# Optimization experiments

Measured on AMD Instinct MI355X. Metric: run time of the kernel, lower is better.

## Reference

```python
import jax, jax.numpy as jnp
import numpy as np

N = 100000      # nodes
E = 1600000     # edges (avg degree 16)
F_IN = 128      # node feature dim
F_OUT = 128     # GCN output dim


def setup_inputs() -> dict:
    key = jax.random.key(0)
    ks = jax.random.split(key, 11)
    s = 0.05  # weight scale to keep activations sane
    return {
        "x": jax.random.normal(ks[0], (N, F_IN), jnp.float32),
        "edge_index": jax.random.randint(ks[1], (2, E), 0, N, jnp.int32),
        "W": jax.random.normal(ks[2], (F_IN, F_OUT), jnp.float32) * s,
        "p": jax.random.normal(ks[3], (F_IN,), jnp.float32),
        "w_ih": jax.random.normal(ks[4], (3 * F_OUT, F_IN), jnp.float32) * s,
        "w_hh": jax.random.normal(ks[5], (3 * F_OUT, F_OUT), jnp.float32) * s,
        "b_ih": jax.random.normal(ks[6], (3 * F_OUT,), jnp.float32) * s,
        "b_hh": jax.random.normal(ks[7], (3 * F_OUT,), jnp.float32) * s,
        "conv_bias": jax.random.normal(ks[8], (F_OUT,), jnp.float32) * s,
        "lin_w": jax.random.normal(ks[9], (1, F_OUT), jnp.float32) * s,
        "lin_b": jax.random.normal(ks[10], (1,), jnp.float32) * s,
    }


def reference(x, edge_index, W, p, w_ih, w_hh, b_ih, b_hh, conv_bias, lin_w, lin_b):
    n_nodes = x.shape[0]
    k, H = W.shape  # k = F_IN rows, H = F_OUT hidden size

    # --- TopK summarize: pick k nodes, gate by tanh(score) -> X_tilde [k, F_IN]
    scores = x @ p / jnp.linalg.norm(p)
    top_vals, top_idx = jax.lax.top_k(scores, k)
    x_tilde = x[top_idx] * jnp.tanh(top_vals)[:, None]

    # --- one GRU step evolving W (hidden state = rows of W)
    gi = x_tilde @ w_ih.T + b_ih   # [k, 3H]
    gh = W @ w_hh.T + b_hh         # [k, 3H]
    r = jax.nn.sigmoid(gi[:, :H] + gh[:, :H])
    z = jax.nn.sigmoid(gi[:, H:2 * H] + gh[:, H:2 * H])
    n = jnp.tanh(gi[:, 2 * H:] + r * gh[:, 2 * H:])
    W_new = (1.0 - z) * n + z * W  # [F_IN, F_OUT]

    # --- GCN conv with fixed W: sym-normalized adjacency with self loops
    row, col = edge_index[0], edge_index[1]
    deg = jax.ops.segment_sum(jnp.ones_like(row, dtype=x.dtype), col,
                              num_segments=n_nodes) + 1.0  # +1 for self loop
    dinv = jax.lax.rsqrt(deg)
    xw = x @ W_new                                   # [N, F_OUT]
    coef = dinv[row] * dinv[col]                     # [E]
    agg = jax.ops.segment_sum(xw[row] * coef[:, None], col, num_segments=n_nodes)
    agg = agg + xw * (dinv * dinv)[:, None] + conv_bias  # self-loop term + bias

    # --- head: ReLU + Linear(F_OUT, 1)
    h = jax.nn.relu(agg)
    return h @ lin_w.T + lin_b  # [N, 1]
```

## Files before the change

kernel.cpp:

```cpp
#include <hip/hip_runtime.h>
#include <math.h>

#define N_NODES 100000
#define N_EDGES 1600000
#define F 128

#define BSH 9
#define NBUCK 196
#define PB_EDGES 4096

typedef unsigned int u32;
typedef unsigned long long u64;
typedef unsigned short u16;
typedef __attribute__((ext_vector_type(8))) short short8;
typedef __attribute__((ext_vector_type(4))) float floatx4;


__device__ __forceinline__ u32 key_of(float s) {
    u32 u = __float_as_uint(s);
    return (u & 0x80000000u) ? ~u : (u | 0x80000000u);
}

__device__ __forceinline__ float wave_reduce(float v) {
    #pragma unroll
    for (int off = 32; off > 0; off >>= 1) v += __shfl_down(v, off, 64);
    return v;
}

__device__ __forceinline__ u16 f2bf(float f) {
    u32 u = __float_as_uint(f);
    u += 0x7fffu + ((u >> 16) & 1u);
    return (u16)(u >> 16);
}


__global__ void k_scores(const float* __restrict__ x, const float* __restrict__ p,
                         float* __restrict__ scores, u32* __restrict__ hist16) {
    int node = blockIdx.x * 4 + (threadIdx.x >> 6);
    int lane = threadIdx.x & 63;
    if (node >= N_NODES) return;
    float2 xv = *(const float2*)&x[(size_t)node * F + lane * 2];
    float2 pv = *(const float2*)&p[lane * 2];
    float d = xv.x * pv.x + xv.y * pv.y;
    d = wave_reduce(d);
    if (lane == 0) {
        scores[node] = d;
        atomicAdd(&hist16[key_of(d) >> 16], 1u);
    }
}


__global__ __launch_bounds__(1024) void k_scan16(const u32* __restrict__ hist16,
                                                 u32* __restrict__ state) {
    __shared__ u32 a[1024];
    int t = threadIdx.x;
    const uint4* h4 = (const uint4*)hist16;
    u32 local = 0;
    #pragma unroll
    for (int i = 0; i < 16; i++) {
        uint4 v = h4[t * 16 + i];
        local += v.x + v.y + v.z + v.w;
    }
    a[t] = local;
    __syncthreads();
    for (int off = 1; off < 1024; off <<= 1) {
        u32 add = (t + off < 1024) ? a[t + off] : 0u;
        __syncthreads();
        a[t] += add;
        __syncthreads();
    }
    u32 S_above = (t == 1023) ? 0u : a[t + 1];
    if (S_above < 128u && a[t] >= 128u) {
        u32 cum = S_above;
        for (int v = t * 64 + 63; v >= t * 64; v--) {
            cum += hist16[v];
            if (cum >= 128u) { state[0] = (u32)v; break; }
        }
    }
}

__global__ void k_collect16(const float* __restrict__ scores, u32* __restrict__ state,
                            u32* __restrict__ cand) {
    u32 T = state[0] << 16;
    int i = blockIdx.x * blockDim.x + threadIdx.x;
    if (i < N_NODES) {
        if (key_of(scores[i]) >= T) {
            u32 pos = atomicAdd(&state[2], 1u);
            if (pos < 2048u) cand[pos] = (u32)i;
        }
    }
}

__global__ void k_assemble16(const float* __restrict__ scores, const float* __restrict__ p,
                             const u32* __restrict__ state, const u32* __restrict__ cand,
                             u32* __restrict__ top_idx, float* __restrict__ gate) {
    __shared__ u32 ci[2048];
    __shared__ float csc[2048];
    __shared__ float s_inv;
    int t = threadIdx.x;
    if (t < 64) {
        float2 pv = *(const float2*)&p[t * 2];
        float d = pv.x * pv.x + pv.y * pv.y;
        d = wave_reduce(d);
        if (t == 0) s_inv = rsqrtf(d);
    }
    u32 nc = state[2]; if (nc > 2048u) nc = 2048u;
    for (u32 i = t; i < nc; i += 256) { u32 ix = cand[i]; ci[i] = ix; csc[i] = scores[ix]; }
    __syncthreads();
    for (u32 i = t; i < nc; i += 256) {
        u32 myk = key_of(csc[i]);
        u32 myi = ci[i];
        int rank = 0;
        for (u32 j = 0; j < nc; j++) {
            u32 ok = key_of(csc[j]);
            rank += (int)((ok > myk) || (ok == myk && ci[j] < myi));
        }
        if (rank < 128) {
            top_idx[rank] = myi;
            gate[rank] = tanhf(csc[i] * s_inv);
        }
    }
}


__global__ __launch_bounds__(256) void k_ggemm(const float* __restrict__ x,
                                               const float* __restrict__ W,
                                               const float* __restrict__ w_ih,
                                               const float* __restrict__ w_hh,
                                               const u32* __restrict__ top_idx,
                                               const float* __restrict__ gate,
                                               float* __restrict__ G) {
    __shared__ float As[32][128];
    __shared__ float Bs[64][131];
    int t = threadIdx.x;
    int k0 = blockIdx.x * 32;
    int by = blockIdx.y;
    int j0 = by * 64;
    bool is_gi = (by < 6);
    #pragma unroll
    for (int i = 0; i < 4; i++) {
        int l = t + i * 256;
        int row = l >> 5, c4 = l & 31;
        float4 v;
        if (is_gi) {
            u32 idx = top_idx[k0 + row];
            float gt = gate[k0 + row];
            v = *(const float4*)&x[(size_t)idx * F + c4 * 4];
            v.x *= gt; v.y *= gt; v.z *= gt; v.w *= gt;
        } else {
            v = *(const float4*)&W[(k0 + row) * F + c4 * 4];
        }
        *(float4*)&As[row][c4 * 4] = v;
    }
    const float* mat = is_gi ? w_ih : w_hh;
    int jbase = is_gi ? j0 : (j0 - 384);
    #pragma unroll
    for (int i = 0; i < 8; i++) {
        int l = t + i * 256;
        int row = l >> 5, c4 = l & 31;
        float4 v = *(const float4*)&mat[(jbase + row) * F + c4 * 4];
        Bs[row][c4 * 4 + 0] = v.x; Bs[row][c4 * 4 + 1] = v.y;
        Bs[row][c4 * 4 + 2] = v.z; Bs[row][c4 * 4 + 3] = v.w;
    }
    __syncthreads();
    int ty = t >> 5, tx = t & 31;
    float acc[4][2] = {};
    #pragma unroll 4
    for (int f = 0; f < 128; f++) {
        float b0 = Bs[tx * 2][f], b1 = Bs[tx * 2 + 1][f];
        #pragma unroll
        for (int i = 0; i < 4; i++) {
            float a = As[ty * 4 + i][f];
            acc[i][0] += a * b0;
            acc[i][1] += a * b1;
        }
    }
    #pragma unroll
    for (int i = 0; i < 4; i++) {
        int k = k0 + ty * 4 + i;
        G[(size_t)k * 768 + j0 + tx * 2 + 0] = acc[i][0];
        G[(size_t)k * 768 + j0 + tx * 2 + 1] = acc[i][1];
    }
}


__global__ void k_gate(const float* __restrict__ G, const float* __restrict__ W,
                       const float* __restrict__ b_ih, const float* __restrict__ b_hh,
                       float* __restrict__ Wnew, u16* __restrict__ Bfrag) {
    int idx = blockIdx.x * blockDim.x + threadIdx.x;
    int k = idx >> 7, h = idx & 127;
    const float* gk = &G[(size_t)k * 768];
    float gir = gk[h]       + b_ih[h];
    float giz = gk[128 + h] + b_ih[128 + h];
    float gin = gk[256 + h] + b_ih[256 + h];
    float ghr = gk[384 + h] + b_hh[h];
    float ghz = gk[512 + h] + b_hh[128 + h];
    float ghn = gk[640 + h] + b_hh[256 + h];
    float wv  = W[k * F + h];
    float rg = 1.0f / (1.0f + expf(-(gir + ghr)));
    float z  = 1.0f / (1.0f + expf(-(giz + ghz)));
    float n  = tanhf(gin + rg * ghn);
    float val = (1.0f - z) * n + z * wv;
    Wnew[k * F + h] = val;
    int nb = h >> 4, kc = k >> 5, q = (k >> 3) & 3, m = h & 15, jj = k & 7;
    Bfrag[(((nb * 4 + kc) * 64) + q * 16 + m) * 8 + jj] = f2bf(val);
}


__global__ void k_bhist(const int* __restrict__ ei, u32* __restrict__ bhist) {
    __shared__ u32 h[NBUCK];
    int t = threadIdx.x;
    for (int i = t; i < NBUCK; i += 256) h[i] = 0u;
    __syncthreads();
    for (int e = blockIdx.x * blockDim.x + t; e < N_EDGES; e += gridDim.x * blockDim.x)
        atomicAdd(&h[((u32)ei[N_EDGES + e]) >> BSH], 1u);
    __syncthreads();
    for (int i = t; i < NBUCK; i += 256) if (h[i]) atomicAdd(&bhist[i], h[i]);
}

__global__ void k_bscan(const u32* __restrict__ bhist, u32* __restrict__ bbase,
                        u32* __restrict__ gcur) {
    __shared__ u32 s[256];
    int t = threadIdx.x;
    u32 v = (t < NBUCK) ? bhist[t] : 0u;
    s[t] = v;
    __syncthreads();
    for (int off = 1; off < 256; off <<= 1) {
        u32 add = (t >= off) ? s[t - off] : 0u;
        __syncthreads();
        s[t] += add;
        __syncthreads();
    }
    u32 excl = s[t] - v;
    if (t < NBUCK) { bbase[t] = excl; gcur[t] = excl; }
    if (t == 0) bbase[NBUCK] = N_EDGES;
}

__global__ void k_part(const int* __restrict__ ei, u32* __restrict__ gcur,
                       u64* __restrict__ pairs) {
    __shared__ u32 lh[NBUCK];
    __shared__ u32 lbase[NBUCK];
    int t = threadIdx.x;
    int e0 = blockIdx.x * PB_EDGES;
    int e1 = e0 + PB_EDGES; if (e1 > N_EDGES) e1 = N_EDGES;
    for (int i = t; i < NBUCK; i += 256) lh[i] = 0u;
    __syncthreads();
    for (int e = e0 + t; e < e1; e += 256)
        atomicAdd(&lh[((u32)ei[N_EDGES + e]) >> BSH], 1u);
    __syncthreads();
    for (int b = t; b < NBUCK; b += 256) {
        u32 c = lh[b];
        lbase[b] = c ? atomicAdd(&gcur[b], c) : 0u;
        lh[b] = 0u;
    }
    __syncthreads();
    for (int e = e0 + t; e < e1; e += 256) {
        u32 d = (u32)ei[N_EDGES + e];
        u32 b = d >> BSH;
        u32 pos = lbase[b] + atomicAdd(&lh[b], 1u);
        pairs[pos] = ((u64)d << 32) | (u32)ei[e];
    }
}

__global__ __launch_bounds__(256) void k_csr(const u64* __restrict__ pairs,
                                             const u32* __restrict__ bbase,
                                             u32* __restrict__ offs,
                                             float* __restrict__ dinv,
                                             u32* __restrict__ ebuf) {
    __shared__ u32 h[512];
    __shared__ u32 sc[512];
    int b = blockIdx.x, t = threadIdx.x;
    u32 lo = (u32)b << BSH;
    u32 base = bbase[b], end = bbase[b + 1];
    for (int i = t; i < 512; i += 256) h[i] = 0u;
    __syncthreads();
    for (u32 i = base + t; i < end; i += 256) {
        u32 dl = (u32)(pairs[i] >> 32) - lo;
        atomicAdd(&h[dl], 1u);
    }
    __syncthreads();
    for (int i = t; i < 512; i += 256) sc[i] = h[i];
    __syncthreads();
    for (int off = 1; off < 512; off <<= 1) {
        int i0 = t, i1 = t + 256;
        u32 v0 = (i0 >= off) ? sc[i0 - off] : 0u;
        u32 v1 = (i1 >= off) ? sc[i1 - off] : 0u;
        __syncthreads();
        sc[i0] += v0; sc[i1] += v1;
        __syncthreads();
    }
    int nn = N_NODES - (int)lo; if (nn > 512) nn = 512;
    for (int i = t; i < nn; i += 256) {
        u32 c = h[i];
        offs[lo + i] = base + (sc[i] - c);
        dinv[lo + i] = rsqrtf((float)c + 1.0f);
    }
    for (int i = t; i < 512; i += 256) sc[i] -= h[i];
    __syncthreads();
    for (u32 i = base + t; i < end; i += 256) {
        u64 pr = pairs[i];
        u32 dl = (u32)(pr >> 32) - lo;
        u32 pos = base + atomicAdd(&sc[dl], 1u);
        ebuf[pos] = (u32)pr;
    }
    if (b == 0 && t == 0) offs[N_NODES] = N_EDGES;
}


__global__ __launch_bounds__(256) void k_gemm(const float* __restrict__ x,
                                              const u16* __restrict__ Bfrag,
                                              u16* __restrict__ xwh) {
    __shared__ __align__(16) u16 As[8192];
    __shared__ __align__(16) u16 Bs[16384];
    int t = threadIdx.x;
    int r0 = blockIdx.x * 64;
    #pragma unroll
    for (int i = 0; i < 8; i++) {
        int l = t + i * 256;
        int row = l >> 5, c4 = l & 31;
        int f0 = c4 * 4;
        float4 v = {0.f, 0.f, 0.f, 0.f};
        if (r0 + row < N_NODES) v = *(const float4*)&x[(size_t)(r0 + row) * F + f0];
        int widx = (((row >> 4) * 4 + (f0 >> 5)) * 64 + ((f0 >> 3) & 3) * 16 + (row & 15)) * 8
                   + (f0 & 7);
        ushort4 s4;
        s4.x = f2bf(v.x); s4.y = f2bf(v.y); s4.z = f2bf(v.z); s4.w = f2bf(v.w);
        *(ushort4*)&As[widx] = s4;
    }
    #pragma unroll
    for (int i = 0; i < 8; i++) {
        int idx = t + i * 256;
        ((uint4*)Bs)[idx] = ((const uint4*)Bfrag)[idx];
    }
    __syncthreads();

    int wv = t >> 6, lane = t & 63;
    floatx4 acc[8] = {};
    #pragma unroll
    for (int kc = 0; kc < 4; kc++) {
        short8 a = *(const short8*)&As[((wv * 4 + kc) * 64 + lane) * 8];
        #pragma unroll
        for (int nb = 0; nb < 8; nb++) {
            short8 b = *(const short8*)&Bs[((nb * 4 + kc) * 64 + lane) * 8];
            acc[nb] = __builtin_amdgcn_mfma_f32_16x16x32_bf16(a, b, acc[nb], 0, 0, 0);
        }
    }
    int q = lane >> 4, m = lane & 15;
    #pragma unroll
    for (int nb = 0; nb < 8; nb++) {
        #pragma unroll
        for (int reg = 0; reg < 4; reg++) {
            int grow = r0 + wv * 16 + q * 4 + reg;
            if (grow < N_NODES)
                xwh[(size_t)grow * F + nb * 16 + m] = f2bf(acc[nb][reg]);
        }
    }
}


__global__ void k_gather(const u32* __restrict__ xw32, const u32* __restrict__ offs,
                         const u32* __restrict__ ebuf, const float* __restrict__ dinv,
                         const float* __restrict__ conv_bias, const float* __restrict__ lin_w,
                         const float* __restrict__ lin_b, float* __restrict__ out) {
    int c = blockIdx.x * 4 + (threadIdx.x >> 6);
    if (c >= N_NODES) return;
    int lane = threadIdx.x & 63;
    u32 jbeg = offs[c], jend = offs[c + 1];
    float ax0 = 0.f, ax1 = 0.f, ax2 = 0.f, ax3 = 0.f;
    float ay0 = 0.f, ay1 = 0.f, ay2 = 0.f, ay3 = 0.f;
    u32 j = jbeg;
    for (; j + 8 <= jend; j += 8) {
        u32 r[8], b[8];
        float w[8];
        #pragma unroll
        for (int i = 0; i < 8; i++) r[i] = ebuf[j + i];
        #pragma unroll
        for (int i = 0; i < 8; i++) w[i] = dinv[r[i]];
        #pragma unroll
        for (int i = 0; i < 8; i++) b[i] = xw32[(size_t)r[i] * 64 + lane];
        ax0 += w[0] * __uint_as_float(b[0] << 16); ay0 += w[0] * __uint_as_float(b[0] & 0xffff0000u);
        ax1 += w[1] * __uint_as_float(b[1] << 16); ay1 += w[1] * __uint_as_float(b[1] & 0xffff0000u);
        ax2 += w[2] * __uint_as_float(b[2] << 16); ay2 += w[2] * __uint_as_float(b[2] & 0xffff0000u);
        ax3 += w[3] * __uint_as_float(b[3] << 16); ay3 += w[3] * __uint_as_float(b[3] & 0xffff0000u);
        ax0 += w[4] * __uint_as_float(b[4] << 16); ay0 += w[4] * __uint_as_float(b[4] & 0xffff0000u);
        ax1 += w[5] * __uint_as_float(b[5] << 16); ay1 += w[5] * __uint_as_float(b[5] & 0xffff0000u);
        ax2 += w[6] * __uint_as_float(b[6] << 16); ay2 += w[6] * __uint_as_float(b[6] & 0xffff0000u);
        ax3 += w[7] * __uint_as_float(b[7] << 16); ay3 += w[7] * __uint_as_float(b[7] & 0xffff0000u);
    }
    for (; j < jend; j++) {
        u32 r = ebuf[j];
        float wv = dinv[r];
        u32 b = xw32[(size_t)r * 64 + lane];
        ax0 += wv * __uint_as_float(b << 16);
        ay0 += wv * __uint_as_float(b & 0xffff0000u);
    }
    float accx = (ax0 + ax1) + (ax2 + ax3);
    float accy = (ay0 + ay1) + (ay2 + ay3);
    float dc = dinv[c];
    u32 sbits = xw32[(size_t)c * 64 + lane];
    float slo = __uint_as_float(sbits << 16);
    float shi = __uint_as_float(sbits & 0xffff0000u);
    accx = dc * accx + dc * dc * slo + conv_bias[lane * 2];
    accy = dc * accy + dc * dc * shi + conv_bias[lane * 2 + 1];
    float hx = fmaxf(accx, 0.f), hy = fmaxf(accy, 0.f);
    float part = hx * lin_w[lane * 2] + hy * lin_w[lane * 2 + 1];
    part = wave_reduce(part);
    if (lane == 0) out[c] = part + lin_b[0];
}


extern "C" void kernel_launch(void* const* d_in, const int* in_sizes, int n_in,
                              void* d_out, int out_size, void* d_ws, size_t ws_size,
                              hipStream_t stream) {
    const float* x         = (const float*)d_in[0];
    const int*   ei        = (const int*)  d_in[1];
    const float* W         = (const float*)d_in[2];
    const float* p         = (const float*)d_in[3];
    const float* w_ih      = (const float*)d_in[4];
    const float* w_hh      = (const float*)d_in[5];
    const float* b_ih      = (const float*)d_in[6];
    const float* b_hh      = (const float*)d_in[7];
    const float* conv_bias = (const float*)d_in[8];
    const float* lin_w     = (const float*)d_in[9];
    const float* lin_b     = (const float*)d_in[10];
    float* out = (float*)d_out;

    u32*   w  = (u32*)d_ws;
    float* wf = (float*)d_ws;

    const size_t SCORES_W = 0;
    const size_t DINV_W   = 100096;
    const size_t OFFS_W   = 200192;
    const size_t HIST16_W = 300288;
    const size_t STATE_W  = 365824;
    const size_t CAND_W   = 365840;
    const size_t TOPI_W   = 367888;
    const size_t GATE_W   = 368016;
    const size_t WNEW_W   = 368144;
    const size_t BFRAG_W  = 384528;
    const size_t BHIST_W  = 392720;
    const size_t BBASE_W  = 392976;
    const size_t GCUR_W   = 393232;
    const size_t PAIRS_W  = 393488;
    const size_t EBUF_W   = 3593488;
    const size_t XW_W     = 5193488;

    float* scores  = wf + SCORES_W;
    float* dinv    = wf + DINV_W;
    u32*   offs    = w  + OFFS_W;
    u32*   hist16  = w  + HIST16_W;
    u32*   state   = w  + STATE_W;
    u32*   cand    = w  + CAND_W;
    u32*   top_idx = w  + TOPI_W;
    float* gate    = wf + GATE_W;
    float* Wnew    = wf + WNEW_W;
    u16*   Bfrag   = (u16*)(w + BFRAG_W);
    u32*   bhist   = w  + BHIST_W;
    u32*   bbase   = w  + BBASE_W;
    u32*   gcur    = w  + GCUR_W;
    u64*   pairs   = (u64*)(w + PAIRS_W);
    float* G       = wf + PAIRS_W;
    u32*   ebuf    = w  + EBUF_W;
    u16*   xwh     = (u16*)(w + XW_W);
    u32*   xw32    = w + XW_W;

    hipMemsetAsync(hist16, 0, (65536 + 8) * sizeof(u32), stream);
    hipMemsetAsync(bhist, 0, NBUCK * sizeof(u32), stream);

    k_scores<<<25000, 256, 0, stream>>>(x, p, scores, hist16);
    k_scan16<<<1, 1024, 0, stream>>>(hist16, state);
    k_collect16<<<392, 256, 0, stream>>>(scores, state, cand);
    k_assemble16<<<1, 256, 0, stream>>>(scores, p, state, cand, top_idx, gate);
    k_ggemm<<<dim3(4, 12), 256, 0, stream>>>(x, W, w_ih, w_hh, top_idx, gate, G);
    k_gate<<<64, 256, 0, stream>>>(G, W, b_ih, b_hh, Wnew, Bfrag);

    k_gemm<<<1563, 256, 0, stream>>>(x, Bfrag, xwh);

    k_bhist<<<392, 256, 0, stream>>>(ei, bhist);
    k_bscan<<<1, 256, 0, stream>>>(bhist, bbase, gcur);
    k_part<<<(N_EDGES + PB_EDGES - 1) / PB_EDGES, 256, 0, stream>>>(ei, gcur, pairs);
    k_csr<<<NBUCK, 256, 0, stream>>>(pairs, bbase, offs, dinv, ebuf);

    k_gather<<<25000, 256, 0, stream>>>(xw32, offs, ebuf, dinv, conv_bias, lin_w,
                                        lin_b, out);
}
```

Before: 363.6 us.

## Pack edge pairs into 32 bits, split gather wave across two edges, merge memsets

Edge partition pairs are now packed into 32 bits (9-bit local destination plus 17-bit source) instead of 64-bit words, halving the traffic of writing and reading the pair buffer in the CSR build. The gather kernel now processes two edges at once per wave, with each half-wave loading 8 bytes per lane per row and the halves combined by a cross-half shuffle. This is meant to issue fewer, wider memory requests. The workspace layout is reordered so the two histogram memsets merge into one call. The packing relies on node ids fitting in 17 bits.

```diff
diff --git a/kernel.cpp b/kernel.cpp
--- a/kernel.cpp
+++ b/kernel.cpp
@@ -10,7 +10,6 @@
 #define PB_EDGES 4096
 
 typedef unsigned int u32;
-typedef unsigned long long u64;
 typedef unsigned short u16;
 typedef __attribute__((ext_vector_type(8))) short short8;
 typedef __attribute__((ext_vector_type(4))) float floatx4;
@@ -32,6 +31,9 @@
     u += 0x7fffu + ((u >> 16) & 1u);
     return (u16)(u >> 16);
 }
+
+__device__ __forceinline__ float bflo(u32 b) { return __uint_as_float(b << 16); }
+__device__ __forceinline__ float bfhi(u32 b) { return __uint_as_float(b & 0xffff0000u); }
 
 
 __global__ void k_scores(const float* __restrict__ x, const float* __restrict__ p,
@@ -237,7 +239,7 @@
 }
 
 __global__ void k_part(const int* __restrict__ ei, u32* __restrict__ gcur,
-                       u64* __restrict__ pairs) {
+                       u32* __restrict__ pairs) {
     __shared__ u32 lh[NBUCK];
     __shared__ u32 lbase[NBUCK];
     int t = threadIdx.x;
@@ -258,11 +260,11 @@
         u32 d = (u32)ei[N_EDGES + e];
         u32 b = d >> BSH;
         u32 pos = lbase[b] + atomicAdd(&lh[b], 1u);
-        pairs[pos] = ((u64)d << 32) | (u32)ei[e];
-    }
-}
-
-__global__ __launch_bounds__(256) void k_csr(const u64* __restrict__ pairs,
+        pairs[pos] = ((d & 511u) << 17) | (u32)ei[e];
+    }
+}
+
+__global__ __launch_bounds__(256) void k_csr(const u32* __restrict__ pairs,
                                              const u32* __restrict__ bbase,
                                              u32* __restrict__ offs,
                                              float* __restrict__ dinv,
@@ -274,10 +276,8 @@
     u32 base = bbase[b], end = bbase[b + 1];
     for (int i = t; i < 512; i += 256) h[i] = 0u;
     __syncthreads();
-    for (u32 i = base + t; i < end; i += 256) {
-        u32 dl = (u32)(pairs[i] >> 32) - lo;
-        atomicAdd(&h[dl], 1u);
-    }
+    for (u32 i = base + t; i < end; i += 256)
+        atomicAdd(&h[pairs[i] >> 17], 1u);
     __syncthreads();
     for (int i = t; i < 512; i += 256) sc[i] = h[i];
     __syncthreads();
@@ -298,10 +298,9 @@
     for (int i = t; i < 512; i += 256) sc[i] -= h[i];
     __syncthreads();
     for (u32 i = base + t; i < end; i += 256) {
-        u64 pr = pairs[i];
-        u32 dl = (u32)(pr >> 32) - lo;
-        u32 pos = base + atomicAdd(&sc[dl], 1u);
-        ebuf[pos] = (u32)pr;
+        u32 pr = pairs[i];
+        u32 pos = base + atomicAdd(&sc[pr >> 17], 1u);
+        ebuf[pos] = pr & 0x1ffffu;
     }
     if (b == 0 && t == 0) offs[N_NODES] = N_EDGES;
 }
@@ -365,45 +364,51 @@
     int c = blockIdx.x * 4 + (threadIdx.x >> 6);
     if (c >= N_NODES) return;
     int lane = threadIdx.x & 63;
+    int half = lane >> 5, sub = lane & 31;
     u32 jbeg = offs[c], jend = offs[c + 1];
-    float ax0 = 0.f, ax1 = 0.f, ax2 = 0.f, ax3 = 0.f;
-    float ay0 = 0.f, ay1 = 0.f, ay2 = 0.f, ay3 = 0.f;
+    float ax = 0.f, ay = 0.f, az = 0.f, aw = 0.f;
     u32 j = jbeg;
     for (; j + 8 <= jend; j += 8) {
-        u32 r[8], b[8];
-        float w[8];
-        #pragma unroll
-        for (int i = 0; i < 8; i++) r[i] = ebuf[j + i];
-        #pragma unroll
-        for (int i = 0; i < 8; i++) w[i] = dinv[r[i]];
-        #pragma unroll
-        for (int i = 0; i < 8; i++) b[i] = xw32[(size_t)r[i] * 64 + lane];
-        ax0 += w[0] * __uint_as_float(b[0] << 16); ay0 += w[0] * __uint_as_float(b[0] & 0xffff0000u);
-        ax1 += w[1] * __uint_as_float(b[1] << 16); ay1 += w[1] * __uint_as_float(b[1] & 0xffff0000u);
-        ax2 += w[2] * __uint_as_float(b[2] << 16); ay2 += w[2] * __uint_as_float(b[2] & 0xffff0000u);
-        ax3 += w[3] * __uint_as_float(b[3] << 16); ay3 += w[3] * __uint_as_float(b[3] & 0xffff0000u);
-        ax0 += w[4] * __uint_as_float(b[4] << 16); ay0 += w[4] * __uint_as_float(b[4] & 0xffff0000u);
-        ax1 += w[5] * __uint_as_float(b[5] << 16); ay1 += w[5] * __uint_as_float(b[5] & 0xffff0000u);
-        ax2 += w[6] * __uint_as_float(b[6] << 16); ay2 += w[6] * __uint_as_float(b[6] & 0xffff0000u);
-        ax3 += w[7] * __uint_as_float(b[7] << 16); ay3 += w[7] * __uint_as_float(b[7] & 0xffff0000u);
-    }
-    for (; j < jend; j++) {
+        u32 r0 = ebuf[j + 0 + half];
+        u32 r1 = ebuf[j + 2 + half];
+        u32 r2 = ebuf[j + 4 + half];
+        u32 r3 = ebuf[j + 6 + half];
+        float w0 = dinv[r0], w1 = dinv[r1], w2 = dinv[r2], w3 = dinv[r3];
+        uint2 b0 = *(const uint2*)&xw32[(size_t)r0 * 64 + sub * 2];
+        uint2 b1 = *(const uint2*)&xw32[(size_t)r1 * 64 + sub * 2];
+        uint2 b2 = *(const uint2*)&xw32[(size_t)r2 * 64 + sub * 2];
+        uint2 b3 = *(const uint2*)&xw32[(size_t)r3 * 64 + sub * 2];
+        ax += w0 * bflo(b0.x); ay += w0 * bfhi(b0.x); az += w0 * bflo(b0.y); aw += w0 * bfhi(b0.y);
+        ax += w1 * bflo(b1.x); ay += w1 * bfhi(b1.x); az += w1 * bflo(b1.y); aw += w1 * bfhi(b1.y);
+        ax += w2 * bflo(b2.x); ay += w2 * bfhi(b2.x); az += w2 * bflo(b2.y); aw += w2 * bfhi(b2.y);
+        ax += w3 * bflo(b3.x); ay += w3 * bfhi(b3.x); az += w3 * bflo(b3.y); aw += w3 * bfhi(b3.y);
+    }
+    for (; j + 2 <= jend; j += 2) {
+        u32 r = ebuf[j + half];
+        float wv = dinv[r];
+        uint2 b = *(const uint2*)&xw32[(size_t)r * 64 + sub * 2];
+        ax += wv * bflo(b.x); ay += wv * bfhi(b.x); az += wv * bflo(b.y); aw += wv * bfhi(b.y);
+    }
+    if (j < jend) {
         u32 r = ebuf[j];
-        float wv = dinv[r];
-        u32 b = xw32[(size_t)r * 64 + lane];
-        ax0 += wv * __uint_as_float(b << 16);
-        ay0 += wv * __uint_as_float(b & 0xffff0000u);
-    }
-    float accx = (ax0 + ax1) + (ax2 + ax3);
-    float accy = (ay0 + ay1) + (ay2 + ay3);
-    float dc = dinv[c];
-    u32 sbits = xw32[(size_t)c * 64 + lane];
-    float slo = __uint_as_float(sbits << 16);
-    float shi = __uint_as_float(sbits & 0xffff0000u);
-    accx = dc * accx + dc * dc * slo + conv_bias[lane * 2];
-    accy = dc * accy + dc * dc * shi + conv_bias[lane * 2 + 1];
-    float hx = fmaxf(accx, 0.f), hy = fmaxf(accy, 0.f);
-    float part = hx * lin_w[lane * 2] + hy * lin_w[lane * 2 + 1];
+        float wv = half ? 0.f : dinv[r];
+        uint2 b = *(const uint2*)&xw32[(size_t)r * 64 + sub * 2];
+        ax += wv * bflo(b.x); ay += wv * bfhi(b.x); az += wv * bflo(b.y); aw += wv * bfhi(b.y);
+    }
+    ax += __shfl_xor(ax, 32, 64);
+    ay += __shfl_xor(ay, 32, 64);
+    az += __shfl_xor(az, 32, 64);
+    aw += __shfl_xor(aw, 32, 64);
+    float dc = dinv[c], d2 = dc * dc;
+    uint2 sb = *(const uint2*)&xw32[(size_t)c * 64 + sub * 2];
+    float4 cb = *(const float4*)&conv_bias[sub * 4];
+    float4 lw = *(const float4*)&lin_w[sub * 4];
+    float h0 = fmaxf(dc * ax + d2 * bflo(sb.x) + cb.x, 0.f);
+    float h1 = fmaxf(dc * ay + d2 * bfhi(sb.x) + cb.y, 0.f);
+    float h2 = fmaxf(dc * az + d2 * bflo(sb.y) + cb.z, 0.f);
+    float h3 = fmaxf(dc * aw + d2 * bfhi(sb.y) + cb.w, 0.f);
+    float part = h0 * lw.x + h1 * lw.y + h2 * lw.z + h3 * lw.w;
+    part = half ? 0.f : part;
     part = wave_reduce(part);
     if (lane == 0) out[c] = part + lin_b[0];
 }
@@ -433,39 +438,38 @@
     const size_t OFFS_W   = 200192;
     const size_t HIST16_W = 300288;
     const size_t STATE_W  = 365824;
-    const size_t CAND_W   = 365840;
-    const size_t TOPI_W   = 367888;
-    const size_t GATE_W   = 368016;
-    const size_t WNEW_W   = 368144;
-    const size_t BFRAG_W  = 384528;
-    const size_t BHIST_W  = 392720;
-    const size_t BBASE_W  = 392976;
-    const size_t GCUR_W   = 393232;
-    const size_t PAIRS_W  = 393488;
-    const size_t EBUF_W   = 3593488;
-    const size_t XW_W     = 5193488;
+    const size_t BHIST_W  = 365832;
+    const size_t CAND_W   = 366080;
+    const size_t TOPI_W   = 368128;
+    const size_t GATE_W   = 368256;
+    const size_t WNEW_W   = 368384;
+    const size_t BFRAG_W  = 384768;
+    const size_t BBASE_W  = 392960;
+    const size_t GCUR_W   = 393216;
+    const size_t PAIRS_W  = 393472;
+    const size_t EBUF_W   = 1993472;
+    const size_t XW_W     = 3593472;
 
     float* scores  = wf + SCORES_W;
     float* dinv    = wf + DINV_W;
     u32*   offs    = w  + OFFS_W;
     u32*   hist16  = w  + HIST16_W;
     u32*   state   = w  + STATE_W;
+    u32*   bhist   = w  + BHIST_W;
     u32*   cand    = w  + CAND_W;
     u32*   top_idx = w  + TOPI_W;
     float* gate    = wf + GATE_W;
     float* Wnew    = wf + WNEW_W;
     u16*   Bfrag   = (u16*)(w + BFRAG_W);
-    u32*   bhist   = w  + BHIST_W;
     u32*   bbase   = w  + BBASE_W;
     u32*   gcur    = w  + GCUR_W;
-    u64*   pairs   = (u64*)(w + PAIRS_W);
+    u32*   pairs   = w  + PAIRS_W;
     float* G       = wf + PAIRS_W;
     u32*   ebuf    = w  + EBUF_W;
     u16*   xwh     = (u16*)(w + XW_W);
     u32*   xw32    = w + XW_W;
 
-    hipMemsetAsync(hist16, 0, (65536 + 8) * sizeof(u32), stream);
-    hipMemsetAsync(bhist, 0, NBUCK * sizeof(u32), stream);
+    hipMemsetAsync(hist16, 0, (65536 + 8 + NBUCK) * sizeof(u32), stream);
 
     k_scores<<<25000, 256, 0, stream>>>(x, p, scores, hist16);
     k_scan16<<<1, 1024, 0, stream>>>(hist16, state);
```

Result: faster. 345.8 us (-4.9%).
